# Performance work log

Hardware: AMD Instinct MI355X
Metric: run time of the kernel (lower is better)

The kernel has to match this reference:

```python
import jax, jax.numpy as jnp
import numpy as np

N_NODES = 50000
N_EDGES = 800000
IN_F = 128
OUT_F = 32
HEADS = 4
EDGE_F = 32  # must equal OUT_F for the original module's shapes to broadcast


def setup_inputs() -> dict:
    key = jax.random.key(0)
    k1, k2, k3, k4, k5, k6, k7 = jax.random.split(key, 7)
    h = jax.random.normal(k1, (N_NODES, IN_F), dtype=jnp.float32)
    edge_indices = jax.random.randint(k2, (2, N_EDGES), 0, N_NODES, dtype=jnp.int32)
    edge_attr = jax.random.normal(k3, (N_EDGES, EDGE_F), dtype=jnp.float32)
    # learned parameters (xavier-ish scaling)
    W = jax.random.normal(k4, (IN_F, HEADS * OUT_F), dtype=jnp.float32) * (1.0 / np.sqrt(IN_F))
    a = jax.random.normal(k5, (HEADS, 2 * OUT_F + EDGE_F), dtype=jnp.float32) * 0.1
    eW = jax.random.normal(k6, (EDGE_F, HEADS * OUT_F), dtype=jnp.float32) * (1.0 / np.sqrt(EDGE_F))
    eb = jnp.zeros((HEADS * OUT_F,), dtype=jnp.float32)
    return {"h": h, "edge_indices": edge_indices, "edge_attr": edge_attr,
            "W": W, "a": a, "eW": eW, "eb": eb}


def reference(h, edge_indices, edge_attr, W, a, eW, eb):
    N = h.shape[0]
    H = a.shape[0]
    F = W.shape[1] // H
    row, col = edge_indices[0], edge_indices[1]

    # node / edge projections
    ht = (h @ W).reshape(N, H, F)                       # [N,H,F]
    et = (edge_attr @ eW + eb).reshape(-1, H, F)        # [E,H,F]

    # split attention vector; avoids materializing the [E,H,3F] concat
    a_i, a_j, a_e = a[:, :F], a[:, F:2 * F], a[:, 2 * F:]
    alpha_i = jnp.einsum('nhf,hf->nh', ht, a_i)         # [N,H]
    alpha_j = jnp.einsum('nhf,hf->nh', ht, a_j)         # [N,H]
    e = alpha_i[row] + alpha_j[col] + jnp.einsum('ehf,hf->eh', et, a_e)  # [E,H]
    e = jax.nn.leaky_relu(e, negative_slope=0.2)

    # scatter-softmax over edges grouped by destination (row), global-max stabilized
    e_exp = jnp.exp(e - jnp.max(e))                     # matches torch exp(e - e.max())
    denom = jax.ops.segment_sum(e_exp, row, num_segments=N)  # [N,H]
    att = e_exp / (denom[row] + 1e-8)                   # [E,H]

    # weighted scatter-add aggregation
    hj = ht[col]                                        # [E,H,F]
    h_out = jax.ops.segment_sum(att[:, :, None] * hj, row, num_segments=N)  # [N,H,F]
    h_out = h_out.reshape(N, H * F)                     # concat=True
    h_out = jax.nn.elu(h_out)                           # dropout=0 (eval)
    return h_out, att
```

## Files before the change

### kernel.cpp

```cpp
#include <hip/hip_runtime.h>
#include <hip/hip_bf16.h>

#define N_NODES 50000
#define N_EDGES 800000
#define IN_F 128
#define OUT_F 32
#define HEADS 4
#define EDGE_F 32
#define HF 128
#define NB 16
#define EB 64
#define SB 256
#define NBLK ((N_NODES + SB - 1) / SB)


__global__ void prep_kernel(const float* __restrict__ eW, const float* __restrict__ eb,
                            const float* __restrict__ a,
                            float* __restrict__ w_eff, float* __restrict__ b_eff) {
    int t = threadIdx.x;
    if (t < 128) {
        int k = t >> 2, h = t & 3;
        float s = 0.f;
        #pragma unroll
        for (int f = 0; f < EDGE_F; ++f)
            s = fmaf(eW[k * HF + h * OUT_F + f], a[h * 96 + 2 * OUT_F + f], s);
        w_eff[k * 4 + h] = s;
    } else if (t < 132) {
        int h = t - 128;
        float s = 0.f;
        #pragma unroll
        for (int f = 0; f < EDGE_F; ++f)
            s = fmaf(eb[h * OUT_F + f], a[h * 96 + 2 * OUT_F + f], s);
        b_eff[h] = s;
    }
}

__global__ __launch_bounds__(256) void node_kernel(
        const float* __restrict__ h, const float* __restrict__ W,
        const float* __restrict__ a,
        __hip_bfloat16* __restrict__ ht_bf,
        float* __restrict__ alpha_i, float* __restrict__ alpha_j) {
    int tid = threadIdx.x;
    int g = tid >> 6, lane = tid & 63;
    int n0 = blockIdx.x * NB;
    __shared__ __align__(16) float hs[NB][IN_F];
    {
        const float4* src = (const float4*)(h + (size_t)n0 * IN_F);
        float4* dst = (float4*)(&hs[0][0]);
        dst[tid] = src[tid];
        dst[tid + 256] = src[tid + 256];
    }
    __syncthreads();
    float acc0[4] = {0.f, 0.f, 0.f, 0.f};
    float acc1[4] = {0.f, 0.f, 0.f, 0.f};
    const float2* Wv = (const float2*)W;
    #pragma unroll 8
    for (int k4 = 0; k4 < IN_F / 4; ++k4) {
        float4 hv[4];
        #pragma unroll
        for (int i = 0; i < 4; ++i)
            hv[i] = *(const float4*)&hs[g * 4 + i][k4 * 4];
        #pragma unroll
        for (int kk = 0; kk < 4; ++kk) {
            float2 w = Wv[(k4 * 4 + kk) * 64 + lane];
            #pragma unroll
            for (int i = 0; i < 4; ++i) {
                float hvv = (&hv[i].x)[kk];
                acc0[i] = fmaf(hvv, w.x, acc0[i]);
                acc1[i] = fmaf(hvv, w.y, acc1[i]);
            }
        }
    }
    int hh = lane >> 4;
    int f0 = (2 * lane) & 31;
    float ai0 = a[hh * 96 + f0],      ai1 = a[hh * 96 + f0 + 1];
    float aj0 = a[hh * 96 + 32 + f0], aj1 = a[hh * 96 + 32 + f0 + 1];
    #pragma unroll
    for (int i = 0; i < 4; ++i) {
        int n = n0 + g * 4 + i;
        *(__hip_bfloat162*)(ht_bf + (size_t)n * HF + 2 * lane) =
            __float22bfloat162_rn(make_float2(acc0[i], acc1[i]));
        float pi = fmaf(acc0[i], ai0, acc1[i] * ai1);
        float pj = fmaf(acc0[i], aj0, acc1[i] * aj1);
        #pragma unroll
        for (int s = 8; s > 0; s >>= 1) {
            pi += __shfl_down(pi, s, 16);
            pj += __shfl_down(pj, s, 16);
        }
        if ((lane & 15) == 0) {
            alpha_i[n * 4 + hh] = pi;
            alpha_j[n * 4 + hh] = pj;
        }
    }
}

__global__ __launch_bounds__(256) void count_kernel(const int* __restrict__ row,
                                                    int* __restrict__ deg) {
    int t = blockIdx.x * 256 + threadIdx.x;
    if (t < N_EDGES / 4) {
        int4 r4 = ((const int4*)row)[t];
        atomicAdd(&deg[r4.x], 1);
        atomicAdd(&deg[r4.y], 1);
        atomicAdd(&deg[r4.z], 1);
        atomicAdd(&deg[r4.w], 1);
    }
}

__device__ __forceinline__ int block_incl_scan(int v, int lane, int wid, int* wsum) {
    int x = v;
    #pragma unroll
    for (int s = 1; s < 64; s <<= 1) {
        int y = __shfl_up(x, s, 64);
        if (lane >= s) x += y;
    }
    if (lane == 63) wsum[wid] = x;
    __syncthreads();
    int add = 0;
    #pragma unroll
    for (int w = 0; w < 4; ++w) add += (w < wid) ? wsum[w] : 0;
    return x + add;
}

__global__ __launch_bounds__(SB) void scan1_kernel(const int* __restrict__ deg,
                                                   int* __restrict__ row_off,
                                                   int* __restrict__ blk_sums) {
    __shared__ int wsum[4];
    int i = blockIdx.x * SB + threadIdx.x;
    int v = (i < N_NODES) ? deg[i] : 0;
    int incl = block_incl_scan(v, threadIdx.x & 63, threadIdx.x >> 6, wsum);
    if (i < N_NODES) row_off[i] = incl - v;
    if (threadIdx.x == SB - 1) blk_sums[blockIdx.x] = incl;
}

__global__ __launch_bounds__(SB) void scan2_kernel(int* __restrict__ blk_sums,
                                                   int* __restrict__ blk_off,
                                                   int* __restrict__ row_off) {
    __shared__ int wsum[4];
    int t = threadIdx.x;
    int v = (t < NBLK) ? blk_sums[t] : 0;
    int incl = block_incl_scan(v, t & 63, t >> 6, wsum);
    if (t < NBLK) blk_off[t] = incl - v;
    if (t == SB - 1) row_off[N_NODES] = incl;
}

__global__ __launch_bounds__(SB) void scan3_kernel(const int* __restrict__ blk_off,
                                                   int* __restrict__ row_off,
                                                   int* __restrict__ cursor) {
    int i = blockIdx.x * SB + threadIdx.x;
    if (i < N_NODES) {
        int v = row_off[i] + blk_off[blockIdx.x];
        row_off[i] = v;
        cursor[i] = v;
    }
}

__global__ __launch_bounds__(256) void edge_kernel(
        const int* __restrict__ row, const int* __restrict__ col,
        const float* __restrict__ ea,
        const float* __restrict__ w_eff, const float* __restrict__ b_eff,
        const float* __restrict__ alpha_i, const float* __restrict__ alpha_j,
        int* __restrict__ cursor, float* __restrict__ rec) {
    __shared__ __align__(16) float eas[EB][EDGE_F + 4];
    __shared__ float wsd[128];
    __shared__ float bs[4];
    int t = threadIdx.x;
    int e0 = blockIdx.x * EB;
    if (t < 128) wsd[t] = w_eff[t];
    if (t < 4) bs[t] = b_eff[t];
    {
        const float4* src = (const float4*)(ea + (size_t)e0 * EDGE_F);
        #pragma unroll
        for (int u = 0; u < 2; ++u) {
            int idx = t + u * 256;
            int i = idx >> 3, f4 = idx & 7;
            ((float4*)&eas[i][0])[f4] = src[idx];
        }
    }
    __syncthreads();
    int i = t >> 2, hh = t & 3;
    int e = e0 + i;
    float s = bs[hh];
    #pragma unroll
    for (int k = 0; k < EDGE_F; ++k) s = fmaf(eas[i][k], wsd[k * 4 + hh], s);
    int r = row[e], c = col[e];
    float ev = s + alpha_i[r * 4 + hh] + alpha_j[c * 4 + hh];
    ev = ev > 0.f ? ev : 0.2f * ev;
    float ex = __expf(ev);
    int pos = 0;
    if (hh == 0) pos = atomicAdd(&cursor[r], 1);
    pos = __shfl(pos, (t & 63) & ~3, 64);
    rec[(size_t)pos * 8 + hh] = ex;
    if (hh == 0)
        *(int2*)(rec + (size_t)pos * 8 + 4) = make_int2(c, e);
}

__global__ __launch_bounds__(256) void agg_kernel(
        const int* __restrict__ row_off, const float* __restrict__ rec,
        const __hip_bfloat16* __restrict__ ht_bf,
        float* __restrict__ hout, float* __restrict__ att) {
    int wave = threadIdx.x >> 6;
    int lane = threadIdx.x & 63;
    int n = blockIdx.x * 4 + wave;
    if (n >= N_NODES) return;
    int beg = row_off[n], end = row_off[n + 1];
    int h2 = lane >> 4;
    float2 acc0 = {0.f, 0.f}, acc1 = {0.f, 0.f};
    float den0 = 0.f, den1 = 0.f;
    int p = beg;
    for (; p + 1 < end; p += 2) {
        const float* rA = rec + (size_t)p * 8;
        const float* rB = rA + 8;
        float exA = rA[h2];
        float exB = rB[h2];
        int cA = *(const int*)(rA + 4);
        int cB = *(const int*)(rB + 4);
        float2 hvA = __bfloat1622float2(
            *(const __hip_bfloat162*)(ht_bf + (size_t)cA * HF + 2 * lane));
        float2 hvB = __bfloat1622float2(
            *(const __hip_bfloat162*)(ht_bf + (size_t)cB * HF + 2 * lane));
        acc0.x = fmaf(exA, hvA.x, acc0.x); acc0.y = fmaf(exA, hvA.y, acc0.y);
        acc1.x = fmaf(exB, hvB.x, acc1.x); acc1.y = fmaf(exB, hvB.y, acc1.y);
        den0 += exA; den1 += exB;
    }
    if (p < end) {
        const float* rA = rec + (size_t)p * 8;
        float exA = rA[h2];
        int cA = *(const int*)(rA + 4);
        float2 hvA = __bfloat1622float2(
            *(const __hip_bfloat162*)(ht_bf + (size_t)cA * HF + 2 * lane));
        acc0.x = fmaf(exA, hvA.x, acc0.x); acc0.y = fmaf(exA, hvA.y, acc0.y);
        den0 += exA;
    }
    float den = den0 + den1;
    float rden = 1.0f / (den + 1e-8f);
    float ox = (acc0.x + acc1.x) * rden, oy = (acc0.y + acc1.y) * rden;
    ox = ox > 0.f ? ox : expm1f(ox);
    oy = oy > 0.f ? oy : expm1f(oy);
    float2 o = {ox, oy};
    ((float2*)(hout + (size_t)n * HF))[lane] = o;
    int h = lane & 3;
    float rden_h = __shfl(rden, h * 16, 64);
    for (int p0 = beg; p0 < end; p0 += 16) {
        int q = p0 + (lane >> 2);
        if (q < end) {
            const float* rQ = rec + (size_t)q * 8;
            int eid = *(const int*)(rQ + 5);
            float ex = rQ[h];
            att[(size_t)eid * 4 + h] = ex * rden_h;
        }
    }
}

extern "C" void kernel_launch(void* const* d_in, const int* in_sizes, int n_in,
                              void* d_out, int out_size, void* d_ws, size_t ws_size,
                              hipStream_t stream) {
    const float* h  = (const float*)d_in[0];
    const int*   ei = (const int*)  d_in[1];
    const float* ea = (const float*)d_in[2];
    const float* W  = (const float*)d_in[3];
    const float* a  = (const float*)d_in[4];
    const float* eW = (const float*)d_in[5];
    const float* eb = (const float*)d_in[6];

    float* out  = (float*)d_out;
    float* hout = out;
    float* att  = out + (size_t)N_NODES * HF;

    char* wsb = (char*)d_ws;
    __hip_bfloat16* ht_bf = (__hip_bfloat16*)wsb;
    float* alpha_i = (float*)(wsb + (size_t)N_NODES * HF * 2);
    float* alpha_j = alpha_i + N_NODES * HEADS;
    float* w_eff   = alpha_j + N_NODES * HEADS;
    float* b_eff   = w_eff + 128;
    int*   deg     = (int*)(b_eff + 4);
    int*   row_off = deg + N_NODES;
    int*   cursor  = row_off + N_NODES + 1;
    int*   blk_sums= cursor + N_NODES;
    int*   blk_off = blk_sums + NBLK;
    float* rec     = (float*)((((uintptr_t)(blk_off + NBLK)) + 31) & ~(uintptr_t)31);

    const int* row = ei;
    const int* col = ei + N_EDGES;

    hipMemsetAsync(deg, 0, (size_t)N_NODES * sizeof(int), stream);

    prep_kernel<<<1, 160, 0, stream>>>(eW, eb, a, w_eff, b_eff);
    node_kernel<<<N_NODES / NB, 256, 0, stream>>>(h, W, a, ht_bf, alpha_i, alpha_j);
    count_kernel<<<(N_EDGES / 4 + 255) / 256, 256, 0, stream>>>(row, deg);
    scan1_kernel<<<NBLK, SB, 0, stream>>>(deg, row_off, blk_sums);
    scan2_kernel<<<1, SB, 0, stream>>>(blk_sums, blk_off, row_off);
    scan3_kernel<<<NBLK, SB, 0, stream>>>(blk_off, row_off, cursor);
    edge_kernel<<<N_EDGES / EB, 256, 0, stream>>>(row, col, ea, w_eff, b_eff,
                                                  alpha_i, alpha_j, cursor, rec);
    agg_kernel<<<(N_NODES + 3) / 4, 256, 0, stream>>>(row_off, rec, ht_bf, hout, att);
}
```

Before: 385.4 us.

## Precompute edge ranks in count pass, pack records to 16B with fp16 exps

The count kernel now stores each edge's atomic return value as its rank within its destination row. The edge kernel can then compute its slot as row_off plus rank without a second atomic cursor pass. The edge kernel is restructured to one thread per edge, computing all four heads with float4 loads. CSR records shrink from 32 to 16 bytes by storing the four exp values as fp16. This cuts scatter and gather traffic at the cost of a rank array and reduced precision in the attention numerators.

```diff
diff --git a/kernel.cpp b/kernel.cpp
--- a/kernel.cpp
+++ b/kernel.cpp
@@ -1,5 +1,6 @@
 #include <hip/hip_runtime.h>
 #include <hip/hip_bf16.h>
+#include <hip/hip_fp16.h>
 
 #define N_NODES 50000
 #define N_EDGES 800000
@@ -9,7 +10,6 @@
 #define EDGE_F 32
 #define HF 128
 #define NB 16
-#define EB 64
 #define SB 256
 #define NBLK ((N_NODES + SB - 1) / SB)
 
@@ -95,14 +95,17 @@
 }
 
 __global__ __launch_bounds__(256) void count_kernel(const int* __restrict__ row,
-                                                    int* __restrict__ deg) {
+                                                    int* __restrict__ deg,
+                                                    int* __restrict__ rank) {
     int t = blockIdx.x * 256 + threadIdx.x;
     if (t < N_EDGES / 4) {
         int4 r4 = ((const int4*)row)[t];
-        atomicAdd(&deg[r4.x], 1);
-        atomicAdd(&deg[r4.y], 1);
-        atomicAdd(&deg[r4.z], 1);
-        atomicAdd(&deg[r4.w], 1);
+        int4 k4;
+        k4.x = atomicAdd(&deg[r4.x], 1);
+        k4.y = atomicAdd(&deg[r4.y], 1);
+        k4.z = atomicAdd(&deg[r4.z], 1);
+        k4.w = atomicAdd(&deg[r4.w], 1);
+        ((int4*)rank)[t] = k4;
     }
 }
 
@@ -144,14 +147,10 @@
 }
 
 __global__ __launch_bounds__(SB) void scan3_kernel(const int* __restrict__ blk_off,
-                                                   int* __restrict__ row_off,
-                                                   int* __restrict__ cursor) {
+                                                   int* __restrict__ row_off) {
     int i = blockIdx.x * SB + threadIdx.x;
-    if (i < N_NODES) {
-        int v = row_off[i] + blk_off[blockIdx.x];
-        row_off[i] = v;
-        cursor[i] = v;
-    }
+    if (i < N_NODES)
+        row_off[i] += blk_off[blockIdx.x];
 }
 
 __global__ __launch_bounds__(256) void edge_kernel(
@@ -159,43 +158,57 @@
         const float* __restrict__ ea,
         const float* __restrict__ w_eff, const float* __restrict__ b_eff,
         const float* __restrict__ alpha_i, const float* __restrict__ alpha_j,
-        int* __restrict__ cursor, float* __restrict__ rec) {
-    __shared__ __align__(16) float eas[EB][EDGE_F + 4];
+        const int* __restrict__ row_off, const int* __restrict__ rank,
+        uint4* __restrict__ rec) {
     __shared__ float wsd[128];
     __shared__ float bs[4];
     int t = threadIdx.x;
-    int e0 = blockIdx.x * EB;
     if (t < 128) wsd[t] = w_eff[t];
     if (t < 4) bs[t] = b_eff[t];
-    {
-        const float4* src = (const float4*)(ea + (size_t)e0 * EDGE_F);
-        #pragma unroll
-        for (int u = 0; u < 2; ++u) {
-            int idx = t + u * 256;
-            int i = idx >> 3, f4 = idx & 7;
-            ((float4*)&eas[i][0])[f4] = src[idx];
-        }
-    }
     __syncthreads();
-    int i = t >> 2, hh = t & 3;
-    int e = e0 + i;
-    float s = bs[hh];
-    #pragma unroll
-    for (int k = 0; k < EDGE_F; ++k) s = fmaf(eas[i][k], wsd[k * 4 + hh], s);
+    int e = blockIdx.x * 256 + t;
+    const float4* src = (const float4*)(ea + (size_t)e * EDGE_F);
+    float4 ev[8];
+    #pragma unroll
+    for (int i = 0; i < 8; ++i) ev[i] = src[i];
     int r = row[e], c = col[e];
-    float ev = s + alpha_i[r * 4 + hh] + alpha_j[c * 4 + hh];
-    ev = ev > 0.f ? ev : 0.2f * ev;
-    float ex = __expf(ev);
-    int pos = 0;
-    if (hh == 0) pos = atomicAdd(&cursor[r], 1);
-    pos = __shfl(pos, (t & 63) & ~3, 64);
-    rec[(size_t)pos * 8 + hh] = ex;
-    if (hh == 0)
-        *(int2*)(rec + (size_t)pos * 8 + 4) = make_int2(c, e);
+    int rk = rank[e];
+    float4 ai = *(const float4*)(alpha_i + (size_t)r * 4);
+    float4 aj = *(const float4*)(alpha_j + (size_t)c * 4);
+    float s0 = bs[0], s1 = bs[1], s2 = bs[2], s3 = bs[3];
+    #pragma unroll
+    for (int i = 0; i < 8; ++i) {
+        #pragma unroll
+        for (int kk = 0; kk < 4; ++kk) {
+            float x = (&ev[i].x)[kk];
+            float4 w4 = *(const float4*)&wsd[(i * 4 + kk) * 4];
+            s0 = fmaf(x, w4.x, s0);
+            s1 = fmaf(x, w4.y, s1);
+            s2 = fmaf(x, w4.z, s2);
+            s3 = fmaf(x, w4.w, s3);
+        }
+    }
+    float e0 = s0 + ai.x + aj.x;
+    float e1 = s1 + ai.y + aj.y;
+    float e2 = s2 + ai.z + aj.z;
+    float e3 = s3 + ai.w + aj.w;
+    e0 = e0 > 0.f ? e0 : 0.2f * e0;
+    e1 = e1 > 0.f ? e1 : 0.2f * e1;
+    e2 = e2 > 0.f ? e2 : 0.2f * e2;
+    e3 = e3 > 0.f ? e3 : 0.2f * e3;
+    __half2 p01 = __floats2half2_rn(__expf(e0), __expf(e1));
+    __half2 p23 = __floats2half2_rn(__expf(e2), __expf(e3));
+    uint4 out;
+    out.x = *reinterpret_cast<unsigned int*>(&p01);
+    out.y = *reinterpret_cast<unsigned int*>(&p23);
+    out.z = (unsigned int)c;
+    out.w = (unsigned int)e;
+    int pos = row_off[r] + rk;
+    rec[pos] = out;
 }
 
 __global__ __launch_bounds__(256) void agg_kernel(
-        const int* __restrict__ row_off, const float* __restrict__ rec,
+        const int* __restrict__ row_off, const uint4* __restrict__ rec,
         const __hip_bfloat16* __restrict__ ht_bf,
         float* __restrict__ hout, float* __restrict__ att) {
     int wave = threadIdx.x >> 6;
@@ -204,16 +217,19 @@
     if (n >= N_NODES) return;
     int beg = row_off[n], end = row_off[n + 1];
     int h2 = lane >> 4;
+    int sh = (h2 & 1) * 16;
     float2 acc0 = {0.f, 0.f}, acc1 = {0.f, 0.f};
     float den0 = 0.f, den1 = 0.f;
     int p = beg;
     for (; p + 1 < end; p += 2) {
-        const float* rA = rec + (size_t)p * 8;
-        const float* rB = rA + 8;
-        float exA = rA[h2];
-        float exB = rB[h2];
-        int cA = *(const int*)(rA + 4);
-        int cB = *(const int*)(rB + 4);
+        uint4 rA = rec[p];
+        uint4 rB = rec[p + 1];
+        unsigned int wA = (h2 & 2) ? rA.y : rA.x;
+        unsigned int wB = (h2 & 2) ? rB.y : rB.x;
+        float exA = __half2float(__ushort_as_half((unsigned short)(wA >> sh)));
+        float exB = __half2float(__ushort_as_half((unsigned short)(wB >> sh)));
+        int cA = (int)rA.z;
+        int cB = (int)rB.z;
         float2 hvA = __bfloat1622float2(
             *(const __hip_bfloat162*)(ht_bf + (size_t)cA * HF + 2 * lane));
         float2 hvB = __bfloat1622float2(
@@ -223,9 +239,10 @@
         den0 += exA; den1 += exB;
     }
     if (p < end) {
-        const float* rA = rec + (size_t)p * 8;
-        float exA = rA[h2];
-        int cA = *(const int*)(rA + 4);
+        uint4 rA = rec[p];
+        unsigned int wA = (h2 & 2) ? rA.y : rA.x;
+        float exA = __half2float(__ushort_as_half((unsigned short)(wA >> sh)));
+        int cA = (int)rA.z;
         float2 hvA = __bfloat1622float2(
             *(const __hip_bfloat162*)(ht_bf + (size_t)cA * HF + 2 * lane));
         acc0.x = fmaf(exA, hvA.x, acc0.x); acc0.y = fmaf(exA, hvA.y, acc0.y);
@@ -243,10 +260,10 @@
     for (int p0 = beg; p0 < end; p0 += 16) {
         int q = p0 + (lane >> 2);
         if (q < end) {
-            const float* rQ = rec + (size_t)q * 8;
-            int eid = *(const int*)(rQ + 5);
-            float ex = rQ[h];
-            att[(size_t)eid * 4 + h] = ex * rden_h;
+            uint4 rQ = rec[q];
+            unsigned int w = (h & 2) ? rQ.y : rQ.x;
+            float ex = __half2float(__ushort_as_half((unsigned short)(w >> ((h & 1) * 16))));
+            att[(size_t)rQ.w * 4 + h] = ex * rden_h;
         }
     }
 }
@@ -274,10 +291,10 @@
     float* b_eff   = w_eff + 128;
     int*   deg     = (int*)(b_eff + 4);
     int*   row_off = deg + N_NODES;
-    int*   cursor  = row_off + N_NODES + 1;
-    int*   blk_sums= cursor + N_NODES;
+    int*   blk_sums= row_off + N_NODES + 1;
     int*   blk_off = blk_sums + NBLK;
-    float* rec     = (float*)((((uintptr_t)(blk_off + NBLK)) + 31) & ~(uintptr_t)31);
+    int*   rank    = (int*)((((uintptr_t)(blk_off + NBLK)) + 15) & ~(uintptr_t)15);
+    uint4* rec     = (uint4*)((((uintptr_t)(rank + N_EDGES)) + 15) & ~(uintptr_t)15);
 
     const int* row = ei;
     const int* col = ei + N_EDGES;
@@ -286,11 +303,11 @@
 
     prep_kernel<<<1, 160, 0, stream>>>(eW, eb, a, w_eff, b_eff);
     node_kernel<<<N_NODES / NB, 256, 0, stream>>>(h, W, a, ht_bf, alpha_i, alpha_j);
-    count_kernel<<<(N_EDGES / 4 + 255) / 256, 256, 0, stream>>>(row, deg);
+    count_kernel<<<(N_EDGES / 4 + 255) / 256, 256, 0, stream>>>(row, deg, rank);
     scan1_kernel<<<NBLK, SB, 0, stream>>>(deg, row_off, blk_sums);
     scan2_kernel<<<1, SB, 0, stream>>>(blk_sums, blk_off, row_off);
-    scan3_kernel<<<NBLK, SB, 0, stream>>>(blk_off, row_off, cursor);
-    edge_kernel<<<N_EDGES / EB, 256, 0, stream>>>(row, col, ea, w_eff, b_eff,
-                                                  alpha_i, alpha_j, cursor, rec);
+    scan3_kernel<<<NBLK, SB, 0, stream>>>(blk_off, row_off);
+    edge_kernel<<<N_EDGES / 256, 256, 0, stream>>>(row, col, ea, w_eff, b_eff,
+                                                   alpha_i, alpha_j, row_off, rank, rec);
     agg_kernel<<<(N_NODES + 3) / 4, 256, 0, stream>>>(row_off, rec, ht_bf, hout, att);
 }
```

Result: no change. 378.9 us (-1.7%).
